# Performance work log

Measured on AMD Instinct MI355X. Metric: run time of the kernel, lower is better.

Reference implementation:

```python
import jax, jax.numpy as jnp
import numpy as np

VOCAB, D, E, B, S = 32000, 1024, 4, 4, 1024
DF = 4 * D  # Expert.internal_dim = d_model * 4


def setup_inputs() -> dict:
    key = jax.random.key(0)
    ks = jax.random.split(key, 14)
    sc = 0.02
    return {
        "tokens": jax.random.randint(ks[0], (B, S), 0, VOCAB),
        "emb": jax.random.normal(ks[1], (VOCAB, D), jnp.float32) * sc,
        "Wih": jax.random.normal(ks[2], (D, D), jnp.float32) * sc,
        "bih": jnp.zeros((D,), jnp.float32),
        "Whh": jax.random.normal(ks[3], (D, D), jnp.float32) * sc,
        "bhh": jnp.zeros((D,), jnp.float32),
        "Wg": jax.random.normal(ks[4], (E, D), jnp.float32) * sc,
        "W1": jax.random.normal(ks[5], (E, D, DF), jnp.float32) * sc,
        "b1": jnp.zeros((E, DF), jnp.float32),
        "W2": jax.random.normal(ks[6], (E, DF, D), jnp.float32) * sc,
        "b2": jnp.zeros((E, D), jnp.float32),
        "Wfc": jax.random.normal(ks[7], (VOCAB, D), jnp.float32) * sc,
        "bfc": jnp.zeros((VOCAB,), jnp.float32),
    }


def reference(tokens, emb, Wih, bih, Whh, bhh, Wg, W1, b1, W2, b2, Wfc, bfc):
    # token embedding: [B,S,D]
    x = emb[tokens]

    # nn.RNN(batch_first=True), tanh nonlinearity, h0 = zeros (h=None path)
    def step(h, xt):
        h = jnp.tanh(xt @ Wih.T + bih + h @ Whh.T + bhh)
        return h, h

    h0 = jnp.zeros((x.shape[0], x.shape[-1]), x.dtype)
    h_last, hs = jax.lax.scan(step, h0, jnp.swapaxes(x, 0, 1))  # hs: [S,B,D]
    x = jnp.swapaxes(hs, 0, 1)  # [B,S,D]

    # DarwinianRouter on pooled sequence repr: softmax gate, top_k=1
    gates = jax.nn.softmax(x.mean(axis=1) @ Wg.T, axis=-1)  # [B,E]
    w, idx = jax.lax.top_k(gates, 1)  # [B,1] each
    idx0 = idx[:, 0]

    # OuroborosMoE dispatch: per-sequence top-1 expert MLP, scaled by gate weight.
    # Gather per-batch expert params instead of boolean-mask gather/scatter loop.
    W1g, b1g = W1[idx0], b1[idx0]          # [B,D,DF], [B,DF]
    W2g, b2g = W2[idx0], b2[idx0]          # [B,DF,D], [B,D]
    h1 = jax.nn.gelu(jnp.einsum('bsd,bdf->bsf', x, W1g) + b1g[:, None, :], approximate=False)
    y = (jnp.einsum('bsf,bfd->bsd', h1, W2g) + b2g[:, None, :]) * w[:, :, None]  # [B,S,D]

    logits = y @ Wfc.T + bfc  # [B,S,VOCAB]
    return logits


if __name__ == "__main__":
    out = reference(**setup_inputs())
    print(out.shape)
```

## Files before the change

### kernel.cpp

```cpp
#include <hip/hip_runtime.h>
#include <hip/hip_bf16.h>
#include <math.h>

#define DD    1024
#define SS    1024
#define BB    4
#define EE    4
#define DFF   4096
#define VOC   32000

typedef __attribute__((ext_vector_type(8))) short v8s;
typedef __attribute__((ext_vector_type(4))) float v4f;

__device__ __forceinline__ unsigned short f2b(float f) {
    unsigned u = __float_as_uint(f);
    unsigned r = (u + 0x7FFFu + ((u >> 16) & 1u)) >> 16;
    return (unsigned short)r;
}

template<int BMODE, int EPI, bool GATHER>
__global__ __launch_bounds__(256)
void gemm_f32(const float* __restrict__ A,
              const int*   __restrict__ gidx,
              const float* __restrict__ Bm,
              const float* __restrict__ bias1,
              const float* __restrict__ bias2,
              float*       __restrict__ C,
              int K, int N)
{
    __shared__ float As[16][68];
    __shared__ float Bs[16][68];

    const int tid = threadIdx.x;
    const int bx = blockIdx.x, by = blockIdx.y;

    const int r  = tid >> 2;
    const int c4 = (tid & 3) * 4;
    const int tx = tid & 15, ty = tid >> 4;

    const float* arow;
    if constexpr (GATHER)
        arow = A + (long long)gidx[by * 64 + r] * K + c4;
    else
        arow = A + (long long)(by * 64 + r) * K + c4;

    const float* brow_bt = Bm + (long long)(bx * 64 + r) * K + c4;

    float acc[4][4] = {};

    for (int k0 = 0; k0 < K; k0 += 16) {
        float4 av = *(const float4*)(arow + k0);
        As[c4 + 0][r] = av.x; As[c4 + 1][r] = av.y;
        As[c4 + 2][r] = av.z; As[c4 + 3][r] = av.w;
        float4 bv = *(const float4*)(brow_bt + k0);
        Bs[c4 + 0][r] = bv.x; Bs[c4 + 1][r] = bv.y;
        Bs[c4 + 2][r] = bv.z; Bs[c4 + 3][r] = bv.w;
        __syncthreads();
        #pragma unroll
        for (int k2 = 0; k2 < 16; ++k2) {
            float4 a = *(const float4*)&As[k2][ty * 4];
            float4 b = *(const float4*)&Bs[k2][tx * 4];
            acc[0][0] += a.x * b.x; acc[0][1] += a.x * b.y; acc[0][2] += a.x * b.z; acc[0][3] += a.x * b.w;
            acc[1][0] += a.y * b.x; acc[1][1] += a.y * b.y; acc[1][2] += a.y * b.z; acc[1][3] += a.y * b.w;
            acc[2][0] += a.z * b.x; acc[2][1] += a.z * b.y; acc[2][2] += a.z * b.z; acc[2][3] += a.z * b.w;
            acc[3][0] += a.w * b.x; acc[3][1] += a.w * b.y; acc[3][2] += a.w * b.z; acc[3][3] += a.w * b.w;
        }
        __syncthreads();
    }

    const int row0 = by * 64 + ty * 4;
    const int col0 = bx * 64 + tx * 4;
    #pragma unroll
    for (int i = 0; i < 4; ++i) {
        float o[4];
        #pragma unroll
        for (int j = 0; j < 4; ++j) {
            int col = col0 + j;
            o[j] = acc[i][j] + bias1[col] + bias2[col];
        }
        *(float4*)(C + (long long)(row0 + i) * N + col0) =
            make_float4(o[0], o[1], o[2], o[3]);
    }
}

__global__ __launch_bounds__(1024)
void rnn_kernel(const float* __restrict__ U,
                const float* __restrict__ Whh,
                float*       __restrict__ HS,
                unsigned long long* __restrict__ hpair)
{
    __shared__ float hs_s[4 * 1088];

    const int tid = threadIdx.x;
    const int g = blockIdx.x;
    const int out = tid >> 4;
    const int chunk = tid & 15;
    const int b = out >> 4;
    const int dl = out & 15;
    const int d_own = g * 16 + dl;
    const bool is_res = (chunk == 0);

    float4 wreg[16];
    #pragma unroll
    for (int j = 0; j < 16; ++j)
        wreg[j] = *(const float4*)(Whh + (size_t)d_own * DD + chunk * 64 + j * 4);

    const int sb = tid >> 8;
    const int sk = (tid & 255) * 4;
    float* sdst = &hs_s[sb * 1088 + sk + ((sk >> 6) << 2)];
    const float* rbase = &hs_s[b * 1088 + chunk * 68];

    for (int t = 0; t < SS; ++t) {
        float u_pre = 0.f;
        if (is_res)
            u_pre = U[((size_t)(b * SS + t)) * DD + d_own];

        if (t > 0) {
            const char* pb = (const char*)(hpair + (size_t)((t - 1) & 1) * 4096)
                             + tid * 32;
            uint4 q0, q1;
            const unsigned tg = (unsigned)t;
            for (;;) {
                asm volatile(
                    "global_load_dwordx4 %0, %2, off sc0 sc1\n\t"
                    "global_load_dwordx4 %1, %2, off offset:16 sc0 sc1\n\t"
                    "s_waitcnt vmcnt(0)"
                    : "=&v"(q0), "=&v"(q1)
                    : "v"(pb)
                    : "memory");
                if ((q0.y == tg) & (q0.w == tg) & (q1.y == tg) & (q1.w == tg))
                    break;
                __builtin_amdgcn_s_sleep(1);
            }
            *(float4*)sdst = make_float4(
                __uint_as_float(q0.x), __uint_as_float(q0.z),
                __uint_as_float(q1.x), __uint_as_float(q1.z));
        }
        __syncthreads();

        float acc = 0.f;
        if (t > 0) {
            #pragma unroll
            for (int j = 0; j < 16; ++j) {
                float4 h4 = *(const float4*)(rbase + j * 4);
                float4 w4 = wreg[j];
                acc += w4.x * h4.x + w4.y * h4.y + w4.z * h4.z + w4.w * h4.w;
            }
            acc += __shfl_xor(acc, 1);
            acc += __shfl_xor(acc, 2);
            acc += __shfl_xor(acc, 4);
            acc += __shfl_xor(acc, 8);
        }

        if (is_res) {
            float h = tanhf(u_pre + acc);
            HS[((size_t)(b * SS + t)) * DD + d_own] = h;
            unsigned long long pk =
                ((unsigned long long)(unsigned)(t + 1) << 32) |
                (unsigned long long)__float_as_uint(h);
            __hip_atomic_store(&hpair[(size_t)(t & 1) * 4096 + b * 1024 + d_own],
                               pk, __ATOMIC_RELAXED, __HIP_MEMORY_SCOPE_AGENT);
        }
        __syncthreads();
    }
}

__global__ __launch_bounds__(256)
void mean_kernel(const float* __restrict__ HS, float* __restrict__ MEANX)
{
    __shared__ float red[4][64];
    const int b = blockIdx.x >> 4, dc = blockIdx.x & 15;
    const int jd = threadIdx.x & 63, sq = threadIdx.x >> 6;
    float acc = 0.f;
    const float* base = HS + (long long)b * SS * DD + dc * 64 + jd;
    for (int s = sq * 256; s < sq * 256 + 256; ++s)
        acc += base[(long long)s * DD];
    red[sq][jd] = acc;
    __syncthreads();
    if (threadIdx.x < 64) {
        float m = red[0][threadIdx.x] + red[1][threadIdx.x] +
                  red[2][threadIdx.x] + red[3][threadIdx.x];
        MEANX[b * DD + dc * 64 + threadIdx.x] = m * (1.0f / (float)SS);
    }
}

__global__ __launch_bounds__(256)
void gate_kernel(const float* __restrict__ MEANX, const float* __restrict__ Wg,
                 float* __restrict__ WGATE, int* __restrict__ IDX)
{
    __shared__ float sc[4][4];
    const int tid = threadIdx.x;
    const int p = tid >> 4, l = tid & 15;
    const int b = p >> 2, e = p & 3;
    float acc = 0.f;
    for (int j = 0; j < 64; ++j)
        acc += MEANX[b * DD + l * 64 + j] * Wg[e * DD + l * 64 + j];
    acc += __shfl_xor(acc, 1); acc += __shfl_xor(acc, 2);
    acc += __shfl_xor(acc, 4); acc += __shfl_xor(acc, 8);
    if (l == 0) sc[b][e] = acc;
    __syncthreads();
    if (tid < 4) {
        float s0 = sc[tid][0], s1 = sc[tid][1], s2 = sc[tid][2], s3 = sc[tid][3];
        float mx = fmaxf(fmaxf(s0, s1), fmaxf(s2, s3));
        float e0 = expf(s0 - mx), e1 = expf(s1 - mx);
        float e2 = expf(s2 - mx), e3 = expf(s3 - mx);
        float inv = 1.0f / (e0 + e1 + e2 + e3);
        float pr[4] = {e0 * inv, e1 * inv, e2 * inv, e3 * inv};
        int arg = 0; float best = pr[0];
        if (pr[1] > best) { best = pr[1]; arg = 1; }
        if (pr[2] > best) { best = pr[2]; arg = 2; }
        if (pr[3] > best) { best = pr[3]; arg = 3; }
        WGATE[tid] = best;
        IDX[tid] = arg;
    }
}

__global__ __launch_bounds__(256)
void cast_kernel(const float* __restrict__ in, unsigned short* __restrict__ out,
                 long long n4)
{
    long long stride = (long long)gridDim.x * blockDim.x;
    for (long long i = (long long)blockIdx.x * blockDim.x + threadIdx.x;
         i < n4; i += stride) {
        float4 v = ((const float4*)in)[i];
        ushort4 o;
        o.x = f2b(v.x); o.y = f2b(v.y); o.z = f2b(v.z); o.w = f2b(v.w);
        ((ushort4*)out)[i] = o;
    }
}

__global__ __launch_bounds__(256)
void transpose_cast(const float* __restrict__ src, const int* __restrict__ expIdx,
                    unsigned short* __restrict__ dst, int R, int C,
                    long long srcExpStride, long long dstZStride)
{
    __shared__ float tbuf[32][33];
    const int tid = threadIdx.x;
    const int z = blockIdx.z;
    const float* S = src + (long long)expIdx[z] * srcExpStride;
    unsigned short* D = dst + (long long)z * dstZStride;
    const int r0 = blockIdx.y * 32, c0 = blockIdx.x * 32;
    const int tr = tid >> 3, tc = (tid & 7) * 4;
    float4 v = *(const float4*)(S + (long long)(r0 + tr) * C + c0 + tc);
    tbuf[tr][tc + 0] = v.x; tbuf[tr][tc + 1] = v.y;
    tbuf[tr][tc + 2] = v.z; tbuf[tr][tc + 3] = v.w;
    __syncthreads();
    ushort4 o;
    o.x = f2b(tbuf[tc + 0][tr]); o.y = f2b(tbuf[tc + 1][tr]);
    o.z = f2b(tbuf[tc + 2][tr]); o.w = f2b(tbuf[tc + 3][tr]);
    *(ushort4*)(D + (long long)(c0 + tr) * R + r0 + tc) = o;
}

__device__ __forceinline__ void load_lds16(const void* g, void* l) {
    __builtin_amdgcn_global_load_lds(
        (const __attribute__((address_space(1))) unsigned int*)g,
        (__attribute__((address_space(3))) unsigned int*)l, 16, 0, 0);
}

template<int EPI>
__global__ __launch_bounds__(256)
void gemm_bf16(const unsigned short* __restrict__ A,
               const unsigned short* __restrict__ Bt,
               const float* __restrict__ bias,
               void* __restrict__ Cv,
               int N, int K,
               long long aStride, long long cStride, long long btStride,
               const float* __restrict__ scaleP, const int* __restrict__ expIdx)
{
    __shared__ __align__(16) unsigned short Asm[128 * 32];
    __shared__ __align__(16) unsigned short Bsm[128 * 32];

    const int tid = threadIdx.x;
    const int wave = tid >> 6, lane = tid & 63;
    const int bm = blockIdx.y * 128, bn = blockIdx.x * 128;
    const int bz = blockIdx.z;
    const int wm = (wave >> 1) * 64, wn = (wave & 1) * 64;
    const int fr = lane & 15, kh = lane >> 4;

    const unsigned short* Az  = A  + (long long)bz * aStride;
    const unsigned short* Btz = Bt + (long long)bz * btStride;
    const float* bp = bias + (expIdx ? (long long)expIdx[bz] * N : 0);

    const int lo0 = wave * 1024 + lane * 16;
    const int lo1 = 4096 + lo0;
    const int r0 = lo0 >> 6, q0 = (lo0 & 63) >> 1;
    const int r1 = lo1 >> 6, q1 = (lo1 & 63) >> 1;
    const unsigned short* a0 = Az  + (size_t)(bm + r0) * K + q0;
    const unsigned short* a1 = Az  + (size_t)(bm + r1) * K + q1;
    const unsigned short* b0 = Btz + (size_t)(bn + r0) * K + q0;
    const unsigned short* b1 = Btz + (size_t)(bn + r1) * K + q1;

    v4f acc[4][4];
    #pragma unroll
    for (int i = 0; i < 4; ++i)
        #pragma unroll
        for (int j = 0; j < 4; ++j) {
            acc[i][j][0] = 0.f; acc[i][j][1] = 0.f;
            acc[i][j][2] = 0.f; acc[i][j][3] = 0.f;
        }

    for (int k0 = 0; k0 < K; k0 += 32) {
        load_lds16(a0 + k0, (char*)Asm + wave * 1024);
        load_lds16(a1 + k0, (char*)Asm + 4096 + wave * 1024);
        load_lds16(b0 + k0, (char*)Bsm + wave * 1024);
        load_lds16(b1 + k0, (char*)Bsm + 4096 + wave * 1024);
        __syncthreads();

        v8s af[4], bfv[4];
        #pragma unroll
        for (int f = 0; f < 4; ++f) {
            af[f]  = *(const v8s*)((const char*)Asm + ((wm + f * 16 + fr) << 6) + (kh << 4));
            bfv[f] = *(const v8s*)((const char*)Bsm + ((wn + f * 16 + fr) << 6) + (kh << 4));
        }
        #pragma unroll
        for (int fi = 0; fi < 4; ++fi)
            #pragma unroll
            for (int fj = 0; fj < 4; ++fj)
                acc[fi][fj] = __builtin_amdgcn_mfma_f32_16x16x32_bf16(
                    af[fi], bfv[fj], acc[fi][fj], 0, 0, 0);
        __syncthreads();
    }

    const float scale = (EPI == 2) ? scaleP[bz] : 1.0f;
    #pragma unroll
    for (int fi = 0; fi < 4; ++fi) {
        #pragma unroll
        for (int fj = 0; fj < 4; ++fj) {
            v4f t = acc[fi][fj];
            int col = bn + wn + fj * 16 + fr;
            float bb = bp[col];
            int rbase = bm + wm + fi * 16 + (kh << 2);
            #pragma unroll
            for (int r = 0; r < 4; ++r) {
                float v = t[r] + bb;
                if constexpr (EPI == 1)
                    v = 0.5f * v * (1.0f + erff(v * 0.70710678118654752440f));
                if constexpr (EPI == 2)
                    v *= scale;
                size_t off = (size_t)bz * (size_t)cStride +
                             (size_t)(rbase + r) * N + col;
                if constexpr (EPI == 0)
                    ((float*)Cv)[off] = v;
                else
                    ((unsigned short*)Cv)[off] = f2b(v);
            }
        }
    }
}

extern "C" void kernel_launch(void* const* d_in, const int* in_sizes, int n_in,
                              void* d_out, int out_size, void* d_ws, size_t ws_size,
                              hipStream_t stream)
{
    const int*   tokens = (const int*)  d_in[0];
    const float* emb    = (const float*)d_in[1];
    const float* Wih    = (const float*)d_in[2];
    const float* bih    = (const float*)d_in[3];
    const float* Whh    = (const float*)d_in[4];
    const float* bhh    = (const float*)d_in[5];
    const float* Wg     = (const float*)d_in[6];
    const float* W1     = (const float*)d_in[7];
    const float* b1     = (const float*)d_in[8];
    const float* W2     = (const float*)d_in[9];
    const float* b2     = (const float*)d_in[10];
    const float* Wfc    = (const float*)d_in[11];
    const float* bfc    = (const float*)d_in[12];
    float* out = (float*)d_out;
    float* ws  = (float*)d_ws;

    float*          U     = ws;
    float*          HS    = ws + 4194304;
    unsigned short* HSbf  = (unsigned short*)(ws + 8388608);
    float*          Ebase = ws + 10485760;
    float*          Fbase = ws + 18874368;
    unsigned short* Ybf   = (unsigned short*)(ws + 27262976);
    float*          MEANX = ws + 29360128;
    float*          WGATE = ws + 29364224;
    int*            IDX   = (int*)(ws + 29364228);
    unsigned long long* HPAIR = (unsigned long long*)Ebase;
    unsigned short* W1T   = (unsigned short*)Ebase;
    unsigned short* W2T   = (unsigned short*)Ebase;
    unsigned short* H1bf  = (unsigned short*)Fbase;
    unsigned short* Wfcbf = (unsigned short*)Ebase;

    hipMemsetAsync(HPAIR, 0, 2 * 4096 * sizeof(unsigned long long), stream);

    gemm_f32<0, 0, true><<<dim3(DD / 64, (BB * SS) / 64, 1), 256, 0, stream>>>(
        emb, tokens, Wih, bih, bhh, U, DD, DD);

    rnn_kernel<<<64, 1024, 0, stream>>>(U, Whh, HS, HPAIR);

    mean_kernel<<<64, 256, 0, stream>>>(HS, MEANX);
    gate_kernel<<<1, 256, 0, stream>>>(MEANX, Wg, WGATE, IDX);

    cast_kernel<<<1024, 256, 0, stream>>>(HS, HSbf, (long long)(BB * SS) * DD / 4);

    transpose_cast<<<dim3(DFF / 32, DD / 32, BB), 256, 0, stream>>>(
        W1, IDX, W1T, DD, DFF, (long long)DD * DFF, (long long)DFF * DD);

    gemm_bf16<1><<<dim3(DFF / 128, SS / 128, BB), 256, 0, stream>>>(
        HSbf, W1T, b1, H1bf, DFF, DD,
        (long long)SS * DD, (long long)SS * DFF, (long long)DFF * DD,
        nullptr, IDX);

    transpose_cast<<<dim3(DD / 32, DFF / 32, BB), 256, 0, stream>>>(
        W2, IDX, W2T, DFF, DD, (long long)DFF * DD, (long long)DD * DFF);

    gemm_bf16<2><<<dim3(DD / 128, SS / 128, BB), 256, 0, stream>>>(
        H1bf, W2T, b2, Ybf, DD, DFF,
        (long long)SS * DFF, (long long)SS * DD, (long long)DD * DFF,
        WGATE, IDX);

    cast_kernel<<<4096, 256, 0, stream>>>(Wfc, (unsigned short*)Wfcbf,
                                          (long long)VOC * DD / 4);

    gemm_bf16<0><<<dim3(VOC / 128, (BB * SS) / 128, 1), 256, 0, stream>>>(
        Ybf, Wfcbf, bfc, out, VOC, DD, 0, 0, 0, nullptr, nullptr);
}
```

Measured before the change: 2.946 ms.

## Use split-bf16 MFMA input GEMM, fuse mean into RNN, swizzle GEMM blocks

Replaces the FP32 SIMT input-projection GEMM with a bf16 MFMA GEMM. It splits each operand into hi and lo bf16 parts and sums three products, which keeps near-fp32 accuracy. The sequence mean is now accumulated inside the RNN kernel, which removes the separate mean pass over HS. The RNN shared-memory buffer is double-buffered by step parity. An XCD-aware block swizzle is added to the bf16 GEMMs to improve L2 locality. This costs extra split-cast kernels and three times the MFMA work on the input GEMM, and the double buffer may let the per-step barrier be relaxed.

```diff
diff --git a/kernel.cpp b/kernel.cpp
--- a/kernel.cpp
+++ b/kernel.cpp
@@ -17,79 +17,49 @@
     unsigned r = (u + 0x7FFFu + ((u >> 16) & 1u)) >> 16;
     return (unsigned short)r;
 }
-
-template<int BMODE, int EPI, bool GATHER>
-__global__ __launch_bounds__(256)
-void gemm_f32(const float* __restrict__ A,
-              const int*   __restrict__ gidx,
-              const float* __restrict__ Bm,
-              const float* __restrict__ bias1,
-              const float* __restrict__ bias2,
-              float*       __restrict__ C,
-              int K, int N)
-{
-    __shared__ float As[16][68];
-    __shared__ float Bs[16][68];
-
-    const int tid = threadIdx.x;
-    const int bx = blockIdx.x, by = blockIdx.y;
-
-    const int r  = tid >> 2;
-    const int c4 = (tid & 3) * 4;
-    const int tx = tid & 15, ty = tid >> 4;
-
-    const float* arow;
+__device__ __forceinline__ float b2f(unsigned short h) {
+    return __uint_as_float((unsigned)h << 16);
+}
+
+__device__ __forceinline__ void xcd_swizzle(int& bx, int& by) {
+    int gx = gridDim.x;
+    int nwg = gx * gridDim.y;
+    int id = by * gx + bx;
+    int q = nwg >> 3, r = nwg & 7;
+    int xcd = id & 7, o = id >> 3;
+    int swz = (xcd < r ? xcd * (q + 1) : r * (q + 1) + (xcd - r) * q) + o;
+    bx = swz % gx; by = swz / gx;
+}
+
+template<bool GATHER>
+__global__ __launch_bounds__(256)
+void split_cast(const float* __restrict__ src, const int* __restrict__ tokens,
+                unsigned short* __restrict__ Xhi, unsigned short* __restrict__ Xlo)
+{
+    const int row = blockIdx.x;
+    const float4* s;
     if constexpr (GATHER)
-        arow = A + (long long)gidx[by * 64 + r] * K + c4;
+        s = (const float4*)(src + (size_t)tokens[row] * DD);
     else
-        arow = A + (long long)(by * 64 + r) * K + c4;
-
-    const float* brow_bt = Bm + (long long)(bx * 64 + r) * K + c4;
-
-    float acc[4][4] = {};
-
-    for (int k0 = 0; k0 < K; k0 += 16) {
-        float4 av = *(const float4*)(arow + k0);
-        As[c4 + 0][r] = av.x; As[c4 + 1][r] = av.y;
-        As[c4 + 2][r] = av.z; As[c4 + 3][r] = av.w;
-        float4 bv = *(const float4*)(brow_bt + k0);
-        Bs[c4 + 0][r] = bv.x; Bs[c4 + 1][r] = bv.y;
-        Bs[c4 + 2][r] = bv.z; Bs[c4 + 3][r] = bv.w;
-        __syncthreads();
-        #pragma unroll
-        for (int k2 = 0; k2 < 16; ++k2) {
-            float4 a = *(const float4*)&As[k2][ty * 4];
-            float4 b = *(const float4*)&Bs[k2][tx * 4];
-            acc[0][0] += a.x * b.x; acc[0][1] += a.x * b.y; acc[0][2] += a.x * b.z; acc[0][3] += a.x * b.w;
-            acc[1][0] += a.y * b.x; acc[1][1] += a.y * b.y; acc[1][2] += a.y * b.z; acc[1][3] += a.y * b.w;
-            acc[2][0] += a.z * b.x; acc[2][1] += a.z * b.y; acc[2][2] += a.z * b.z; acc[2][3] += a.z * b.w;
-            acc[3][0] += a.w * b.x; acc[3][1] += a.w * b.y; acc[3][2] += a.w * b.z; acc[3][3] += a.w * b.w;
-        }
-        __syncthreads();
-    }
-
-    const int row0 = by * 64 + ty * 4;
-    const int col0 = bx * 64 + tx * 4;
-    #pragma unroll
-    for (int i = 0; i < 4; ++i) {
-        float o[4];
-        #pragma unroll
-        for (int j = 0; j < 4; ++j) {
-            int col = col0 + j;
-            o[j] = acc[i][j] + bias1[col] + bias2[col];
-        }
-        *(float4*)(C + (long long)(row0 + i) * N + col0) =
-            make_float4(o[0], o[1], o[2], o[3]);
-    }
+        s = (const float4*)(src + (size_t)row * DD);
+    const int c = threadIdx.x;
+    float4 v = s[c];
+    ushort4 hi, lo;
+    hi.x = f2b(v.x); hi.y = f2b(v.y); hi.z = f2b(v.z); hi.w = f2b(v.w);
+    lo.x = f2b(v.x - b2f(hi.x)); lo.y = f2b(v.y - b2f(hi.y));
+    lo.z = f2b(v.z - b2f(hi.z)); lo.w = f2b(v.w - b2f(hi.w));
+    ((ushort4*)Xhi)[(size_t)row * 256 + c] = hi;
+    ((ushort4*)Xlo)[(size_t)row * 256 + c] = lo;
 }
 
 __global__ __launch_bounds__(1024)
 void rnn_kernel(const float* __restrict__ U,
                 const float* __restrict__ Whh,
                 float*       __restrict__ HS,
-                unsigned long long* __restrict__ hpair)
-{
-    __shared__ float hs_s[4 * 1088];
+                unsigned long long* __restrict__ hpair,
+                float*       __restrict__ MEANX)
+{
+    __shared__ float hs_s[2][4 * 1088];
 
     const int tid = threadIdx.x;
     const int g = blockIdx.x;
@@ -107,14 +77,17 @@
 
     const int sb = tid >> 8;
     const int sk = (tid & 255) * 4;
-    float* sdst = &hs_s[sb * 1088 + sk + ((sk >> 6) << 2)];
-    const float* rbase = &hs_s[b * 1088 + chunk * 68];
+    const int sks = sk + ((sk >> 6) << 2);
+    const int rofs = b * 1088 + chunk * 68;
+
+    float m_acc = 0.f;
 
     for (int t = 0; t < SS; ++t) {
         float u_pre = 0.f;
         if (is_res)
             u_pre = U[((size_t)(b * SS + t)) * DD + d_own];
 
+        const int par = t & 1;
         if (t > 0) {
             const char* pb = (const char*)(hpair + (size_t)((t - 1) & 1) * 4096)
                              + tid * 32;
@@ -132,7 +105,7 @@
                     break;
                 __builtin_amdgcn_s_sleep(1);
             }
-            *(float4*)sdst = make_float4(
+            *(float4*)&hs_s[par][sb * 1088 + sks] = make_float4(
                 __uint_as_float(q0.x), __uint_as_float(q0.z),
                 __uint_as_float(q1.x), __uint_as_float(q1.z));
         }
@@ -140,6 +113,7 @@
 
         float acc = 0.f;
         if (t > 0) {
+            const float* rbase = &hs_s[par][rofs];
             #pragma unroll
             for (int j = 0; j < 16; ++j) {
                 float4 h4 = *(const float4*)(rbase + j * 4);
@@ -155,33 +129,17 @@
         if (is_res) {
             float h = tanhf(u_pre + acc);
             HS[((size_t)(b * SS + t)) * DD + d_own] = h;
+            m_acc += h;
             unsigned long long pk =
                 ((unsigned long long)(unsigned)(t + 1) << 32) |
                 (unsigned long long)__float_as_uint(h);
             __hip_atomic_store(&hpair[(size_t)(t & 1) * 4096 + b * 1024 + d_own],
                                pk, __ATOMIC_RELAXED, __HIP_MEMORY_SCOPE_AGENT);
         }
-        __syncthreads();
-    }
-}
-
-__global__ __launch_bounds__(256)
-void mean_kernel(const float* __restrict__ HS, float* __restrict__ MEANX)
-{
-    __shared__ float red[4][64];
-    const int b = blockIdx.x >> 4, dc = blockIdx.x & 15;
-    const int jd = threadIdx.x & 63, sq = threadIdx.x >> 6;
-    float acc = 0.f;
-    const float* base = HS + (long long)b * SS * DD + dc * 64 + jd;
-    for (int s = sq * 256; s < sq * 256 + 256; ++s)
-        acc += base[(long long)s * DD];
-    red[sq][jd] = acc;
-    __syncthreads();
-    if (threadIdx.x < 64) {
-        float m = red[0][threadIdx.x] + red[1][threadIdx.x] +
-                  red[2][threadIdx.x] + red[3][threadIdx.x];
-        MEANX[b * DD + dc * 64 + threadIdx.x] = m * (1.0f / (float)SS);
-    }
+    }
+
+    if (is_res)
+        MEANX[b * DD + d_own] = m_acc * (1.0f / (float)SS);
 }
 
 __global__ __launch_bounds__(256)
@@ -272,7 +230,9 @@
 
     const int tid = threadIdx.x;
     const int wave = tid >> 6, lane = tid & 63;
-    const int bm = blockIdx.y * 128, bn = blockIdx.x * 128;
+    int bxs = blockIdx.x, bys = blockIdx.y;
+    xcd_swizzle(bxs, bys);
+    const int bm = bys * 128, bn = bxs * 128;
     const int bz = blockIdx.z;
     const int wm = (wave >> 1) * 64, wn = (wave & 1) * 64;
     const int fr = lane & 15, kh = lane >> 4;
@@ -348,6 +308,101 @@
     }
 }
 
+__global__ __launch_bounds__(256)
+void gemm_bf16_split(const unsigned short* __restrict__ Ahi,
+                     const unsigned short* __restrict__ Alo,
+                     const unsigned short* __restrict__ Bhi,
+                     const unsigned short* __restrict__ Blo,
+                     const float* __restrict__ bias1,
+                     const float* __restrict__ bias2,
+                     float* __restrict__ C, int N, int K)
+{
+    __shared__ __align__(16) unsigned short AsmH[128 * 32];
+    __shared__ __align__(16) unsigned short AsmL[128 * 32];
+    __shared__ __align__(16) unsigned short BsmH[128 * 32];
+    __shared__ __align__(16) unsigned short BsmL[128 * 32];
+
+    const int tid = threadIdx.x;
+    const int wave = tid >> 6, lane = tid & 63;
+    int bxs = blockIdx.x, bys = blockIdx.y;
+    xcd_swizzle(bxs, bys);
+    const int bm = bys * 128, bn = bxs * 128;
+    const int wm = (wave >> 1) * 64, wn = (wave & 1) * 64;
+    const int fr = lane & 15, kh = lane >> 4;
+
+    const int lo0 = wave * 1024 + lane * 16;
+    const int lo1 = 4096 + lo0;
+    const int r0 = lo0 >> 6, q0 = (lo0 & 63) >> 1;
+    const int r1 = lo1 >> 6, q1 = (lo1 & 63) >> 1;
+    const unsigned short* ah0 = Ahi + (size_t)(bm + r0) * K + q0;
+    const unsigned short* ah1 = Ahi + (size_t)(bm + r1) * K + q1;
+    const unsigned short* al0 = Alo + (size_t)(bm + r0) * K + q0;
+    const unsigned short* al1 = Alo + (size_t)(bm + r1) * K + q1;
+    const unsigned short* bh0 = Bhi + (size_t)(bn + r0) * K + q0;
+    const unsigned short* bh1 = Bhi + (size_t)(bn + r1) * K + q1;
+    const unsigned short* bl0 = Blo + (size_t)(bn + r0) * K + q0;
+    const unsigned short* bl1 = Blo + (size_t)(bn + r1) * K + q1;
+
+    v4f acc[4][4];
+    #pragma unroll
+    for (int i = 0; i < 4; ++i)
+        #pragma unroll
+        for (int j = 0; j < 4; ++j) {
+            acc[i][j][0] = 0.f; acc[i][j][1] = 0.f;
+            acc[i][j][2] = 0.f; acc[i][j][3] = 0.f;
+        }
+
+    for (int k0 = 0; k0 < K; k0 += 32) {
+        load_lds16(ah0 + k0, (char*)AsmH + wave * 1024);
+        load_lds16(ah1 + k0, (char*)AsmH + 4096 + wave * 1024);
+        load_lds16(al0 + k0, (char*)AsmL + wave * 1024);
+        load_lds16(al1 + k0, (char*)AsmL + 4096 + wave * 1024);
+        load_lds16(bh0 + k0, (char*)BsmH + wave * 1024);
+        load_lds16(bh1 + k0, (char*)BsmH + 4096 + wave * 1024);
+        load_lds16(bl0 + k0, (char*)BsmL + wave * 1024);
+        load_lds16(bl1 + k0, (char*)BsmL + 4096 + wave * 1024);
+        __syncthreads();
+
+        v8s ahf[4], alf[4];
+        #pragma unroll
+        for (int f = 0; f < 4; ++f) {
+            int ao = ((wm + f * 16 + fr) << 6) + (kh << 4);
+            ahf[f] = *(const v8s*)((const char*)AsmH + ao);
+            alf[f] = *(const v8s*)((const char*)AsmL + ao);
+        }
+        #pragma unroll
+        for (int fj = 0; fj < 4; ++fj) {
+            int bo = ((wn + fj * 16 + fr) << 6) + (kh << 4);
+            v8s bh = *(const v8s*)((const char*)BsmH + bo);
+            v8s bl = *(const v8s*)((const char*)BsmL + bo);
+            #pragma unroll
+            for (int fi = 0; fi < 4; ++fi) {
+                acc[fi][fj] = __builtin_amdgcn_mfma_f32_16x16x32_bf16(
+                    alf[fi], bh, acc[fi][fj], 0, 0, 0);
+                acc[fi][fj] = __builtin_amdgcn_mfma_f32_16x16x32_bf16(
+                    ahf[fi], bl, acc[fi][fj], 0, 0, 0);
+                acc[fi][fj] = __builtin_amdgcn_mfma_f32_16x16x32_bf16(
+                    ahf[fi], bh, acc[fi][fj], 0, 0, 0);
+            }
+        }
+        __syncthreads();
+    }
+
+    #pragma unroll
+    for (int fi = 0; fi < 4; ++fi) {
+        #pragma unroll
+        for (int fj = 0; fj < 4; ++fj) {
+            v4f t = acc[fi][fj];
+            int col = bn + wn + fj * 16 + fr;
+            float bb = bias1[col] + bias2[col];
+            int rbase = bm + wm + fi * 16 + (kh << 2);
+            #pragma unroll
+            for (int r = 0; r < 4; ++r)
+                C[(size_t)(rbase + r) * N + col] = t[r] + bb;
+        }
+    }
+}
+
 extern "C" void kernel_launch(void* const* d_in, const int* in_sizes, int n_in,
                               void* d_out, int out_size, void* d_ws, size_t ws_size,
                               hipStream_t stream)
@@ -377,7 +432,11 @@
     float*          MEANX = ws + 29360128;
     float*          WGATE = ws + 29364224;
     int*            IDX   = (int*)(ws + 29364228);
-    unsigned long long* HPAIR = (unsigned long long*)Ebase;
+    unsigned short* Xhi   = (unsigned short*)Ebase;
+    unsigned short* Xlo   = (unsigned short*)(Ebase + 2097152);
+    unsigned short* Whi   = (unsigned short*)(Ebase + 4194304);
+    unsigned short* Wlo   = (unsigned short*)(Ebase + 4718592);
+    unsigned long long* HPAIR = (unsigned long long*)Fbase;
     unsigned short* W1T   = (unsigned short*)Ebase;
     unsigned short* W2T   = (unsigned short*)Ebase;
     unsigned short* H1bf  = (unsigned short*)Fbase;
@@ -385,12 +444,14 @@
 
     hipMemsetAsync(HPAIR, 0, 2 * 4096 * sizeof(unsigned long long), stream);
 
-    gemm_f32<0, 0, true><<<dim3(DD / 64, (BB * SS) / 64, 1), 256, 0, stream>>>(
-        emb, tokens, Wih, bih, bhh, U, DD, DD);
-
-    rnn_kernel<<<64, 1024, 0, stream>>>(U, Whh, HS, HPAIR);
-
-    mean_kernel<<<64, 256, 0, stream>>>(HS, MEANX);
+    split_cast<true ><<<BB * SS, 256, 0, stream>>>(emb, tokens, Xhi, Xlo);
+    split_cast<false><<<DD, 256, 0, stream>>>(Wih, nullptr, Whi, Wlo);
+
+    gemm_bf16_split<<<dim3(DD / 128, (BB * SS) / 128, 1), 256, 0, stream>>>(
+        Xhi, Xlo, Whi, Wlo, bih, bhh, U, DD, DD);
+
+    rnn_kernel<<<64, 1024, 0, stream>>>(U, Whh, HS, HPAIR, MEANX);
+
     gate_kernel<<<1, 256, 0, stream>>>(MEANX, Wg, WGATE, IDX);
 
     cast_kernel<<<1024, 256, 0, stream>>>(HS, HSbf, (long long)(BB * SS) * DD / 4);
@@ -411,8 +472,7 @@
         (long long)SS * DFF, (long long)SS * DD, (long long)DD * DFF,
         WGATE, IDX);
 
-    cast_kernel<<<4096, 256, 0, stream>>>(Wfc, (unsigned short*)Wfcbf,
-                                          (long long)VOC * DD / 4);
+    cast_kernel<<<4096, 256, 0, stream>>>(Wfc, Wfcbf, (long long)VOC * DD / 4);
 
     gemm_bf16<0><<<dim3(VOC / 128, (BB * SS) / 128, 1), 256, 0, stream>>>(
         Ybf, Wfcbf, bfc, out, VOC, DD, 0, 0, 0, nullptr, nullptr);
```

After: 2.824 ms. 1.04x faster.
